# Optimization experiments

Hardware: AMD Instinct MI355X
Metric: run time of the kernel (lower is better)

## Reference

```python
import jax, jax.numpy as jnp
import numpy as np
import math

NUM_HEADS = 16
NUM_BUCKETS = 32
MAX_DISTANCE = 128
ALPHA = 32.0


def _rel_bucket(rel_pos):
    # bidirectional T5-style bucketing
    nb = NUM_BUCKETS // 2
    buckets = (rel_pos > 0).astype(jnp.int32) * nb
    rel_pos = jnp.abs(rel_pos)
    max_exact = nb // 2
    is_small = rel_pos < max_exact
    large = max_exact + (
        jnp.log(rel_pos.astype(jnp.float32) / max_exact + 1e-06)
        / math.log(MAX_DISTANCE / max_exact)
        * (nb - max_exact)
    ).astype(jnp.int32)
    large = jnp.minimum(large, nb - 1)
    return buckets + jnp.where(is_small, rel_pos, large)


def setup_inputs() -> dict:
    key = jax.random.key(0)
    ks = jax.random.split(key, 12)
    T, B, E = 1024, 4, 1024
    hd = E // NUM_HEADS
    s = 0.02
    f32 = jnp.float32
    return {
        "query": jax.random.normal(ks[0], (T, B, E), f32),
        "q_w": jax.random.normal(ks[1], (E, E), f32) * s,
        "q_b": jnp.zeros((E,), f32),
        "k_w": jax.random.normal(ks[2], (E, E), f32) * s,
        "k_b": jnp.zeros((E,), f32),
        "v_w": jax.random.normal(ks[3], (E, E), f32) * s,
        "v_b": jnp.zeros((E,), f32),
        "out_w": jax.random.normal(ks[4], (E, E), f32) * s,
        "out_b": jnp.zeros((E,), f32),
        "rel_emb": jax.random.normal(ks[5], (NUM_BUCKETS, NUM_HEADS), f32) * 0.1,
        "grep_w": jax.random.normal(ks[6], (hd, 8), f32) * s,
        "grep_b": jnp.zeros((8,), f32),
        "grep_a": jnp.ones((1, NUM_HEADS, 1, 1), f32),
        "bias_k": jax.random.normal(ks[7], (1, 1, E), f32) * s,
        "bias_v": jax.random.normal(ks[8], (1, 1, E), f32) * s,
    }


def reference(query, q_w, q_b, k_w, k_b, v_w, v_b, out_w, out_b,
              rel_emb, grep_w, grep_b, grep_a, bias_k, bias_v):
    tgt_len, bsz, embed_dim = query.shape
    nh = NUM_HEADS
    hd = embed_dim // nh
    scaling = hd ** (-0.5)

    # projections (self-attention: q, k, v all from query)
    q = query @ q_w + q_b
    k = query @ k_w + k_b
    v = query @ v_w + v_b
    q = q * scaling / ALPHA

    # bias_kv concat along sequence axis
    k = jnp.concatenate([k, jnp.tile(bias_k, (1, bsz, 1))], axis=0)
    v = jnp.concatenate([v, jnp.tile(bias_v, (1, bsz, 1))], axis=0)

    # faithful to source layout (including its (bsz,tgt,nh,hd)->(bsz*nh,tgt,hd) reshape)
    q = jnp.transpose(q.reshape(tgt_len, bsz, nh, hd), (1, 0, 2, 3)).reshape(bsz * nh, tgt_len, hd)
    k = jnp.transpose(k.reshape(-1, bsz, nh, hd), (1, 0, 2, 3)).reshape(bsz * nh, -1, hd)
    v = jnp.transpose(v.reshape(-1, bsz, nh, hd), (1, 0, 2, 3)).reshape(bsz * nh, -1, hd)
    src_len = k.shape[1]

    # [B*H, T, S]
    attn_weights = jnp.einsum("bth,bsh->bts", q, k)

    # T5-style relative position bias
    rel_pos = jnp.arange(src_len)[None, :] - jnp.arange(tgt_len)[:, None]
    buckets = _rel_bucket(rel_pos)                        # [T, S]
    pb = rel_emb[buckets]                                 # [T, S, H]
    pb = jnp.transpose(pb, (2, 0, 1))                     # [H, T, S]
    pb = jnp.tile(pb[None], (bsz, 1, 1, 1)).reshape(bsz * nh, tgt_len, src_len)

    # GRU-style gating of the position bias
    query_layer = q.reshape(bsz, nh, tgt_len, hd) * ALPHA / scaling
    gate = jax.nn.sigmoid((query_layer @ grep_w + grep_b).sum(-1, keepdims=True))
    gate = (gate * grep_a).reshape(bsz * nh, tgt_len, 1)
    attn_weights = attn_weights + gate * pb

    probs = jax.nn.softmax(attn_weights, axis=-1)
    attn = jnp.einsum("bts,bsh->bth", probs, v)           # [B*H, T, hd]
    attn = attn.reshape(bsz, nh, tgt_len, hd)
    attn = jnp.transpose(attn, (2, 0, 1, 3)).reshape(tgt_len, bsz, embed_dim)
    return attn @ out_w + out_b
```

## Files before the change

kernel.cpp:

```cpp
#include <hip/hip_runtime.h>
#include <stdint.h>

typedef unsigned short u16;
typedef unsigned int   u32;
typedef __attribute__((ext_vector_type(4)))  float f32x4;
typedef __attribute__((ext_vector_type(16))) float f32x16;
typedef __attribute__((ext_vector_type(8)))  short short8;
typedef __attribute__((ext_vector_type(8)))  u16   u16x8;
typedef __attribute__((ext_vector_type(4)))  u16   u16x4;
typedef __attribute__((ext_vector_type(4)))  u32   u32x4;
typedef __attribute__((ext_vector_type(4)))  float fv4;

#define T_LEN 1024
#define EMB   1024
#define SPAD  1088
#define LOG2E 1.44269504f

#define OFF_QX   (0ull)
#define OFF_VT   (0ull)
#define OFF_WT   (8912896ull)
#define OFF_QB   (17301504ull)
#define OFF_KB   (25690112ull)
#define OFF_VB   (34603008ull)
#define OFF_AT   (34603008ull)
#define OFF_GATE (43515904ull)
#define OFF_PB   (43778048ull)
#define OFF_AUX  (43909120ull)

__device__ __forceinline__ u16 f2bf(float f) {
  uint32_t u = __builtin_bit_cast(uint32_t, f);
  u += 0x7FFFu + ((u >> 16) & 1u);
  return (u16)(u >> 16);
}
__device__ __forceinline__ float bf2f(u16 s) {
  uint32_t u = ((uint32_t)s) << 16;
  return __builtin_bit_cast(float, u);
}
__device__ __forceinline__ void gld_lds16(const void* gp, void* lp) {
  __builtin_amdgcn_global_load_lds(
      (const __attribute__((address_space(1))) uint32_t*)(uintptr_t)(gp),
      (__attribute__((address_space(3))) uint32_t*)(uintptr_t)(lp),
      16, 0, 0);
}

__global__ void k_convert_q(const float* __restrict__ q, u16* __restrict__ qx) {
  int i = blockIdx.x * 256 + threadIdx.x;
  fv4 v = *((const fv4*)q + i);
  u16x4 o = { f2bf(v[0]), f2bf(v[1]), f2bf(v[2]), f2bf(v[3]) };
  *((u16x4*)qx + i) = o;
}

__global__ void k_transw(const float* __restrict__ w0, const float* __restrict__ w1,
                         const float* __restrict__ w2, const float* __restrict__ w3,
                         u16* __restrict__ wt) {
  __shared__ float tile[32][33];
  const int z = blockIdx.z;
  const float* w = (z == 0) ? w0 : (z == 1) ? w1 : (z == 2) ? w2 : w3;
  const int r0 = blockIdx.y * 32, c0 = blockIdx.x * 32;
  const int tx = threadIdx.x, ty = threadIdx.y;
  #pragma unroll
  for (int j = 0; j < 32; j += 8)
    tile[ty + j][tx] = w[(size_t)(r0 + ty + j) * EMB + c0 + tx];
  __syncthreads();
  u16* o = wt + (size_t)z * EMB * EMB;
  #pragma unroll
  for (int j = 0; j < 32; j += 8)
    o[(size_t)(c0 + ty + j) * EMB + r0 + tx] = f2bf(tile[tx][ty + j]);
}

__global__ void k_pb(const float* __restrict__ rel_emb, float* __restrict__ pbtab,
                     const float* __restrict__ grep_w, const float* __restrict__ grep_b,
                     float* __restrict__ aux) {
  int i = blockIdx.x * 256 + threadIdx.x;
  int rel = 1024 - i;
  int bucket = (rel > 0) ? 16 : 0;
  int r = rel < 0 ? -rel : rel;
  int bidx;
  if (r < 8) bidx = r;
  else {
    float lf = __logf((float)r / 8.0f + 1e-6f) * (1.0f / logf(16.0f)) * 8.0f;
    int large = 8 + (int)lf;
    bidx = large < 15 ? large : 15;
  }
  bucket += bidx;
  #pragma unroll
  for (int h = 0; h < 16; ++h) pbtab[h * 2048 + i] = rel_emb[bucket * 16 + h] * LOG2E;
  if (blockIdx.x == 0) {
    if (threadIdx.x < 64) {
      float s = 0.f;
      #pragma unroll
      for (int j = 0; j < 8; ++j) s += grep_w[threadIdx.x * 8 + j];
      aux[threadIdx.x] = s;
    } else if (threadIdx.x == 64) {
      float s = 0.f;
      #pragma unroll
      for (int j = 0; j < 8; ++j) s += grep_b[j];
      aux[64] = s;
    }
  }
}

__device__ __forceinline__ void gemm_tile(const u16* __restrict__ A, const u16* __restrict__ Bt,
                                          int m0, int n0, u16* As, u16* Bs, f32x4 acc[4][4]) {
  const int tid = threadIdx.x;
  const int lane = tid & 63, wid = tid >> 6;
  const int wm = wid >> 1, wn = wid & 1;
  const int l15 = lane & 15, l4 = lane >> 4;
  for (int kt = 0; kt < EMB; kt += 32) {
    #pragma unroll
    for (int i = 0; i < 2; ++i) {
      int cw = wid * 64 + i * 256;
      int c = cw + lane;
      int row = c >> 2, cb = c & 3;
      gld_lds16(A  + (size_t)(m0 + row) * EMB + kt + cb * 8, (char*)As + (size_t)cw * 16);
      gld_lds16(Bt + (size_t)(n0 + row) * EMB + kt + cb * 8, (char*)Bs + (size_t)cw * 16);
    }
    __syncthreads();
    short8 a[4], b[4];
    #pragma unroll
    for (int f = 0; f < 4; ++f) {
      a[f] = *(const short8*)(As + (wm * 64 + f * 16 + l15) * 32 + l4 * 8);
      b[f] = *(const short8*)(Bs + (wn * 64 + f * 16 + l15) * 32 + l4 * 8);
    }
    #pragma unroll
    for (int mi = 0; mi < 4; ++mi)
      #pragma unroll
      for (int ni = 0; ni < 4; ++ni)
        acc[mi][ni] = __builtin_amdgcn_mfma_f32_16x16x32_bf16(a[mi], b[ni], acc[mi][ni], 0, 0, 0);
    __syncthreads();
  }
}

__global__ __launch_bounds__(256, 2) void k_qkv_gemm(const u16* __restrict__ qx, const u16* __restrict__ wt,
    const float* __restrict__ qbias, const float* __restrict__ kbias, const float* __restrict__ vbias,
    u16* __restrict__ qb, u16* __restrict__ kb, u16* __restrict__ vb) {
  __shared__ u16 lds[8192];
  f32x4 acc[4][4];
  #pragma unroll
  for (int i = 0; i < 4; ++i)
    #pragma unroll
    for (int j = 0; j < 4; ++j) acc[i][j] = (f32x4){0.f, 0.f, 0.f, 0.f};
  const int m0 = blockIdx.y * 128, n0g = blockIdx.x * 128;
  gemm_tile(qx, wt, m0, n0g, lds, lds + 4096, acc);
  const int z = n0g >> 10;
  const float* bias = (z == 0) ? qbias : (z == 1) ? kbias : vbias;
  const int lane = threadIdx.x & 63, wid = threadIdx.x >> 6;
  const int wm = wid >> 1, wn = wid & 1, l15 = lane & 15, l4 = lane >> 4;
  #pragma unroll
  for (int ni = 0; ni < 4; ++ni) {
    int colg = n0g + wn * 64 + ni * 16 + l15;
    int col = colg & 1023;
    float bv = bias[col];
    int h = col >> 6, d = col & 63;
    #pragma unroll
    for (int mi = 0; mi < 4; ++mi) {
      #pragma unroll
      for (int r = 0; r < 4; ++r) {
        int row = m0 + wm * 64 + mi * 16 + l4 * 4 + r;
        int t = row >> 2, b = row & 3;
        float v = acc[mi][ni][r] + bv;
        if (z == 0) {
          int x = b * 16 + (t >> 6), u = ((t & 63) << 4) + h;
          qb[((size_t)x * 1024 + u) * 64 + d] = f2bf(v * (LOG2E / 256.0f));
        } else {
          int w = t * 16 + h;
          int j = w / 1025;
          int u = w - j * 1025;
          int x = b * 16 + j;
          if (z == 1) kb[((size_t)x * SPAD + u) * 64 + d] = f2bf(v);
          else        vb[((size_t)x * SPAD + u) * 64 + d] = f2bf(v);
        }
      }
    }
  }
}

__global__ void k_biaskv(const float* __restrict__ bias_k, const float* __restrict__ bias_v,
                         u16* __restrict__ kb, u16* __restrict__ vb) {
  int i = blockIdx.x * 256 + threadIdx.x;
  int b = i >> 10, h = (i >> 6) & 15, d = i & 63;
  int x = b * 16 + 15, u = 1009 + h;
  kb[((size_t)x * SPAD + u) * 64 + d] = f2bf(bias_k[h * 64 + d]);
  vb[((size_t)x * SPAD + u) * 64 + d] = f2bf(bias_v[h * 64 + d]);
}

__global__ void k_vtrans(const u16* __restrict__ vb, u16* __restrict__ vt) {
  __shared__ u16 t[64][72];
  const int x = blockIdx.y;
  const int u0 = blockIdx.x * 64;
  const int tid = threadIdx.x;
  const int ur = tid >> 2, c0 = (tid & 3) * 16;
  const u16* src = vb + ((size_t)x * SPAD + u0 + ur) * 64 + c0;
  u16x8 a0 = *(const u16x8*)(src);
  u16x8 a1 = *(const u16x8*)(src + 8);
  *(u16x8*)(&t[ur][c0]) = a0;
  *(u16x8*)(&t[ur][c0 + 8]) = a1;
  __syncthreads();
  const int d = tid >> 2, j = tid & 3;
  u16x8 o0, o1;
  #pragma unroll
  for (int i = 0; i < 8; ++i) o0[i] = t[j * 16 + i][d];
  #pragma unroll
  for (int i = 0; i < 8; ++i) o1[i] = t[j * 16 + 8 + i][d];
  u16* dst = vt + ((size_t)x * 64 + d) * SPAD + u0 + j * 16;
  *(u16x8*)(dst) = o0;
  *(u16x8*)(dst + 8) = o1;
}

__global__ void k_gate(const u16* __restrict__ qb, const float* __restrict__ aux,
                       const float* __restrict__ grep_a, float* __restrict__ gate) {
  int tid = threadIdx.x, lane = tid & 63, wid = tid >> 6;
  int row0 = (blockIdx.x * 4 + wid) * 8;
  int sub = lane >> 3, d0 = (lane & 7) * 8;
  int item = row0 + sub;
  u16x8 q8 = *(const u16x8*)(qb + (size_t)item * 64 + d0);
  float acc = 0.f;
  #pragma unroll
  for (int j = 0; j < 8; ++j) acc += bf2f(q8[j]) * aux[d0 + j];
  acc += __shfl_xor(acc, 1);
  acc += __shfl_xor(acc, 2);
  acc += __shfl_xor(acc, 4);
  if ((lane & 7) == 0) {
    float v = acc * (256.0f / LOG2E) + aux[64];
    float s = 1.0f / (1.0f + __expf(-v));
    gate[item] = s * grep_a[(item >> 10) & 15];
  }
}

__global__ __launch_bounds__(256, 2) void k_attn(const u16* __restrict__ qb, const u16* __restrict__ kb,
    const u16* __restrict__ vt, const float* __restrict__ gate, const float* __restrict__ pbt,
    u16* __restrict__ at) {
  __shared__ float pb_s[2048];
  const int tid = threadIdx.x, lane = tid & 63, wid = tid >> 6;
  const int l31 = lane & 31, l5 = lane >> 5;
  const int bid = blockIdx.x;
  const int x = (bid & 7) + ((bid >> 6) << 3);
  const int tblk = (bid >> 3) & 7;
  const int h = x & 15, b = x >> 4;
  const int T = tblk * 128 + wid * 32 + l31;

  #pragma unroll
  for (int i = 0; i < 2; ++i) {
    int idx = (tid + i * 256) * 4;
    *(fv4*)(pb_s + idx) = *(const fv4*)(pbt + (size_t)h * 2048 + idx);
  }

  short8 qf[4];
  #pragma unroll
  for (int c = 0; c < 4; ++c)
    qf[c] = *(const short8*)(qb + ((size_t)x * 1024 + T) * 64 + c * 16 + l5 * 8);
  const float g = gate[(size_t)x * 1024 + T];

  const u16* kbx = kb + (size_t)x * SPAD * 64;
  const u16* vtx = vt + (size_t)x * 64 * SPAD;

  f32x16 O0 = {}, O1 = {};
  float lsum = 0.f;
  __syncthreads();

  for (int ic = 0; ic < 16; ++ic) {
    const int s0 = ic * 64;
    short8 ka[2][4];
    #pragma unroll
    for (int ss = 0; ss < 2; ++ss)
      #pragma unroll
      for (int c = 0; c < 4; ++c)
        ka[ss][c] = *(const short8*)(kbx + (size_t)(s0 + ss * 32 + l31) * 64 + c * 16 + l5 * 8);
    f32x16 sc0 = {}, sc1 = {};
    #pragma unroll
    for (int c = 0; c < 4; ++c) {
      sc0 = __builtin_amdgcn_mfma_f32_32x32x16_bf16(ka[0][c], qf[c], sc0, 0, 0, 0);
      sc1 = __builtin_amdgcn_mfma_f32_32x32x16_bf16(ka[1][c], qf[c], sc1, 0, 0, 0);
    }
    short8 va[2][4];
    #pragma unroll
    for (int ds = 0; ds < 2; ++ds)
      #pragma unroll
      for (int c = 0; c < 4; ++c)
        va[ds][c] = *(const short8*)(vtx + (size_t)(ds * 32 + l31) * SPAD + s0 + c * 16 + l5 * 8);

    const int base = 1024 + T - s0;
    u32 pk[16];
    #pragma unroll
    for (int r = 0; r < 16; r += 2) {
      int soff = (r & 3) + 8 * (r >> 2) + 4 * l5;
      float p0 = exp2f(sc0[r]     + g * pb_s[base - soff]);
      float p1 = exp2f(sc0[r + 1] + g * pb_s[base - soff - 1]);
      lsum += p0 + p1;
      pk[r >> 1] = (__builtin_bit_cast(u32, p1) & 0xFFFF0000u) |
                   (__builtin_bit_cast(u32, p0) >> 16);
    }
    #pragma unroll
    for (int r = 0; r < 16; r += 2) {
      int soff = 32 + (r & 3) + 8 * (r >> 2) + 4 * l5;
      float p0 = exp2f(sc1[r]     + g * pb_s[base - soff]);
      float p1 = exp2f(sc1[r + 1] + g * pb_s[base - soff - 1]);
      lsum += p0 + p1;
      pk[8 + (r >> 1)] = (__builtin_bit_cast(u32, p1) & 0xFFFF0000u) |
                         (__builtin_bit_cast(u32, p0) >> 16);
    }

    const bool lo = (l5 == 0);
    #pragma unroll
    for (int ss = 0; ss < 2; ++ss) {
      u32 X0 = (u32)__shfl_xor((int)pk[ss * 8 + 0], 32);
      u32 X1 = (u32)__shfl_xor((int)pk[ss * 8 + 1], 32);
      u32 X2 = (u32)__shfl_xor((int)pk[ss * 8 + 2], 32);
      u32 X3 = (u32)__shfl_xor((int)pk[ss * 8 + 3], 32);
      u32x4 f0 = { lo ? pk[ss * 8 + 0] : X2, lo ? pk[ss * 8 + 1] : X3,
                   lo ? X0 : pk[ss * 8 + 2], lo ? X1 : pk[ss * 8 + 3] };
      short8 pf0 = __builtin_bit_cast(short8, f0);
      O0 = __builtin_amdgcn_mfma_f32_32x32x16_bf16(va[0][ss * 2], pf0, O0, 0, 0, 0);
      O1 = __builtin_amdgcn_mfma_f32_32x32x16_bf16(va[1][ss * 2], pf0, O1, 0, 0, 0);
      u32 Y0 = (u32)__shfl_xor((int)pk[ss * 8 + 4], 32);
      u32 Y1 = (u32)__shfl_xor((int)pk[ss * 8 + 5], 32);
      u32 Y2 = (u32)__shfl_xor((int)pk[ss * 8 + 6], 32);
      u32 Y3 = (u32)__shfl_xor((int)pk[ss * 8 + 7], 32);
      u32x4 f1 = { lo ? pk[ss * 8 + 4] : Y2, lo ? pk[ss * 8 + 5] : Y3,
                   lo ? Y0 : pk[ss * 8 + 6], lo ? Y1 : pk[ss * 8 + 7] };
      short8 pf1 = __builtin_bit_cast(short8, f1);
      O0 = __builtin_amdgcn_mfma_f32_32x32x16_bf16(va[0][ss * 2 + 1], pf1, O0, 0, 0, 0);
      O1 = __builtin_amdgcn_mfma_f32_32x32x16_bf16(va[1][ss * 2 + 1], pf1, O1, 0, 0, 0);
    }
  }

  float dot = 0.f;
  #pragma unroll
  for (int c = 0; c < 4; ++c) {
    short8 kt = *(const short8*)(kbx + (size_t)1024 * 64 + c * 16 + l5 * 8);
    #pragma unroll
    for (int j = 0; j < 8; ++j)
      dot += bf2f((u16)qf[c][j]) * bf2f((u16)kt[j]);
  }
  dot += __shfl_xor(dot, 32);
  float se = dot + g * pb_s[T];
  float p_t = exp2f(se);
  lsum += __shfl_xor(lsum, 32);
  float linv = 1.0f / (lsum + p_t);

  #pragma unroll
  for (int ds = 0; ds < 2; ++ds) {
    #pragma unroll
    for (int q2 = 0; q2 < 4; ++q2) {
      int d0 = ds * 32 + q2 * 8 + l5 * 4;
      u16x4 ov;
      #pragma unroll
      for (int e = 0; e < 4; ++e) {
        float vtl = bf2f(vtx[(size_t)(d0 + e) * SPAD + 1024]);
        float o = ((ds ? O1[q2 * 4 + e] : O0[q2 * 4 + e]) + p_t * vtl) * linv;
        ov[e] = f2bf(o);
      }
      *(u16x4*)(at + ((size_t)(T * 4 + b)) * 1024 + h * 64 + d0) = ov;
    }
  }
}

__global__ __launch_bounds__(256, 2) void k_out_gemm(const u16* __restrict__ at, const u16* __restrict__ wt3,
                                                     const float* __restrict__ obias, float* __restrict__ out) {
  __shared__ u16 lds[8192];
  f32x4 acc[4][4];
  #pragma unroll
  for (int i = 0; i < 4; ++i)
    #pragma unroll
    for (int j = 0; j < 4; ++j) acc[i][j] = (f32x4){0.f, 0.f, 0.f, 0.f};
  const int m0 = blockIdx.y * 128, n0 = blockIdx.x * 128;
  gemm_tile(at, wt3, m0, n0, lds, lds + 4096, acc);
  const int lane = threadIdx.x & 63, wid = threadIdx.x >> 6;
  const int wm = wid >> 1, wn = wid & 1, l15 = lane & 15, l4 = lane >> 4;
  #pragma unroll
  for (int ni = 0; ni < 4; ++ni) {
    int col = n0 + wn * 64 + ni * 16 + l15;
    float bv = obias[col];
    #pragma unroll
    for (int mi = 0; mi < 4; ++mi) {
      #pragma unroll
      for (int r = 0; r < 4; ++r) {
        int row = m0 + wm * 64 + mi * 16 + l4 * 4 + r;
        out[(size_t)row * 1024 + col] = acc[mi][ni][r] + bv;
      }
    }
  }
}

extern "C" void kernel_launch(void* const* d_in, const int* in_sizes, int n_in,
                              void* d_out, int out_size, void* d_ws, size_t ws_size,
                              hipStream_t stream) {
  const float* query   = (const float*)d_in[0];
  const float* q_w     = (const float*)d_in[1];
  const float* q_b     = (const float*)d_in[2];
  const float* k_w     = (const float*)d_in[3];
  const float* k_b     = (const float*)d_in[4];
  const float* v_w     = (const float*)d_in[5];
  const float* v_b     = (const float*)d_in[6];
  const float* out_w   = (const float*)d_in[7];
  const float* out_b   = (const float*)d_in[8];
  const float* rel_emb = (const float*)d_in[9];
  const float* grep_w  = (const float*)d_in[10];
  const float* grep_b  = (const float*)d_in[11];
  const float* grep_a  = (const float*)d_in[12];
  const float* bias_k  = (const float*)d_in[13];
  const float* bias_v  = (const float*)d_in[14];
  char* ws = (char*)d_ws;
  u16*   qx  = (u16*)(ws + OFF_QX);
  u16*   vt  = (u16*)(ws + OFF_VT);
  u16*   wt  = (u16*)(ws + OFF_WT);
  u16*   qb  = (u16*)(ws + OFF_QB);
  u16*   kb  = (u16*)(ws + OFF_KB);
  u16*   vb  = (u16*)(ws + OFF_VB);
  u16*   at  = (u16*)(ws + OFF_AT);
  float* gate = (float*)(ws + OFF_GATE);
  float* pbt  = (float*)(ws + OFF_PB);
  float* aux  = (float*)(ws + OFF_AUX);
  float* out  = (float*)d_out;

  k_convert_q<<<dim3(4096), dim3(256), 0, stream>>>(query, qx);
  k_transw<<<dim3(32, 32, 4), dim3(32, 8), 0, stream>>>(q_w, k_w, v_w, out_w, wt);
  k_pb<<<dim3(8), dim3(256), 0, stream>>>(rel_emb, pbt, grep_w, grep_b, aux);
  k_qkv_gemm<<<dim3(24, 32), dim3(256), 0, stream>>>(qx, wt, q_b, k_b, v_b, qb, kb, vb);
  k_biaskv<<<dim3(16), dim3(256), 0, stream>>>(bias_k, bias_v, kb, vb);
  k_vtrans<<<dim3(17, 64), dim3(256), 0, stream>>>(vb, vt);
  k_gate<<<dim3(2048), dim3(256), 0, stream>>>(qb, aux, grep_a, gate);
  k_attn<<<dim3(512), dim3(256), 0, stream>>>(qb, kb, vt, gate, pbt, at);
  k_out_gemm<<<dim3(8, 32), dim3(256), 0, stream>>>(at, wt + (size_t)3 * EMB * EMB, out_b, out);
}
```

Baseline: 248.9 us.

## Merge prep and mid kernels, prefetch K in attention, use permlane32 swap

Three small setup kernels are merged into one launch, and bias_kv insertion, V transpose and gate computation are merged into another, which cuts the launch count from nine to five. The attention loop now double-buffers K fragments so the next chunk's loads are issued ahead of the current MFMAs. It also wraps the MFMA sections in s_setprio and replaces the shfl_xor-plus-select exchange with v_permlane32_swap. The trade-off is higher register pressure from the prefetch buffers, plus a bias_v overwrite that now depends on an index range inside the transpose.

```diff
diff --git a/kernel.cpp b/kernel.cpp
--- a/kernel.cpp
+++ b/kernel.cpp
@@ -43,59 +43,61 @@
       16, 0, 0);
 }
 
-__global__ void k_convert_q(const float* __restrict__ q, u16* __restrict__ qx) {
-  int i = blockIdx.x * 256 + threadIdx.x;
-  fv4 v = *((const fv4*)q + i);
-  u16x4 o = { f2bf(v[0]), f2bf(v[1]), f2bf(v[2]), f2bf(v[3]) };
-  *((u16x4*)qx + i) = o;
-}
-
-__global__ void k_transw(const float* __restrict__ w0, const float* __restrict__ w1,
-                         const float* __restrict__ w2, const float* __restrict__ w3,
-                         u16* __restrict__ wt) {
+__global__ void k_prep(const float* __restrict__ q, u16* __restrict__ qx,
+                       const float* __restrict__ w0, const float* __restrict__ w1,
+                       const float* __restrict__ w2, const float* __restrict__ w3,
+                       u16* __restrict__ wt,
+                       const float* __restrict__ rel_emb, float* __restrict__ pbtab,
+                       const float* __restrict__ grep_w, const float* __restrict__ grep_b,
+                       float* __restrict__ aux) {
   __shared__ float tile[32][33];
-  const int z = blockIdx.z;
-  const float* w = (z == 0) ? w0 : (z == 1) ? w1 : (z == 2) ? w2 : w3;
-  const int r0 = blockIdx.y * 32, c0 = blockIdx.x * 32;
-  const int tx = threadIdx.x, ty = threadIdx.y;
-  #pragma unroll
-  for (int j = 0; j < 32; j += 8)
-    tile[ty + j][tx] = w[(size_t)(r0 + ty + j) * EMB + c0 + tx];
-  __syncthreads();
-  u16* o = wt + (size_t)z * EMB * EMB;
-  #pragma unroll
-  for (int j = 0; j < 32; j += 8)
-    o[(size_t)(c0 + ty + j) * EMB + r0 + tx] = f2bf(tile[tx][ty + j]);
-}
-
-__global__ void k_pb(const float* __restrict__ rel_emb, float* __restrict__ pbtab,
-                     const float* __restrict__ grep_w, const float* __restrict__ grep_b,
-                     float* __restrict__ aux) {
-  int i = blockIdx.x * 256 + threadIdx.x;
-  int rel = 1024 - i;
-  int bucket = (rel > 0) ? 16 : 0;
-  int r = rel < 0 ? -rel : rel;
-  int bidx;
-  if (r < 8) bidx = r;
-  else {
-    float lf = __logf((float)r / 8.0f + 1e-6f) * (1.0f / logf(16.0f)) * 8.0f;
-    int large = 8 + (int)lf;
-    bidx = large < 15 ? large : 15;
-  }
-  bucket += bidx;
-  #pragma unroll
-  for (int h = 0; h < 16; ++h) pbtab[h * 2048 + i] = rel_emb[bucket * 16 + h] * LOG2E;
-  if (blockIdx.x == 0) {
-    if (threadIdx.x < 64) {
-      float s = 0.f;
-      #pragma unroll
-      for (int j = 0; j < 8; ++j) s += grep_w[threadIdx.x * 8 + j];
-      aux[threadIdx.x] = s;
-    } else if (threadIdx.x == 64) {
-      float s = 0.f;
-      #pragma unroll
-      for (int j = 0; j < 8; ++j) s += grep_b[j];
-      aux[64] = s;
+  const int bid = blockIdx.x, tid = threadIdx.x;
+  if (bid < 4096) {
+    int i = bid * 256 + tid;
+    fv4 v = *((const fv4*)q + i);
+    u16x4 o = { f2bf(v[0]), f2bf(v[1]), f2bf(v[2]), f2bf(v[3]) };
+    *((u16x4*)qx + i) = o;
+  } else if (bid < 8192) {
+    int b2 = bid - 4096;
+    int z = b2 >> 10, xy = b2 & 1023;
+    int r0 = (xy >> 5) * 32, c0 = (xy & 31) * 32;
+    const float* w = (z == 0) ? w0 : (z == 1) ? w1 : (z == 2) ? w2 : w3;
+    int tx = tid & 31, ty = tid >> 5;
+    #pragma unroll
+    for (int j = 0; j < 32; j += 8)
+      tile[ty + j][tx] = w[(size_t)(r0 + ty + j) * EMB + c0 + tx];
+    __syncthreads();
+    u16* o = wt + (size_t)z * EMB * EMB;
+    #pragma unroll
+    for (int j = 0; j < 32; j += 8)
+      o[(size_t)(c0 + ty + j) * EMB + r0 + tx] = f2bf(tile[tx][ty + j]);
+  } else {
+    int i = (bid - 8192) * 256 + tid;
+    int rel = 1024 - i;
+    int bucket = (rel > 0) ? 16 : 0;
+    int r = rel < 0 ? -rel : rel;
+    int bidx;
+    if (r < 8) bidx = r;
+    else {
+      float lf = __logf((float)r / 8.0f + 1e-6f) * (1.0f / logf(16.0f)) * 8.0f;
+      int large = 8 + (int)lf;
+      bidx = large < 15 ? large : 15;
+    }
+    bucket += bidx;
+    #pragma unroll
+    for (int hh = 0; hh < 16; ++hh) pbtab[hh * 2048 + i] = rel_emb[bucket * 16 + hh] * LOG2E;
+    if (bid == 8192) {
+      if (tid < 64) {
+        float s = 0.f;
+        #pragma unroll
+        for (int j = 0; j < 8; ++j) s += grep_w[tid * 8 + j];
+        aux[tid] = s;
+      } else if (tid == 64) {
+        float s = 0.f;
+        #pragma unroll
+        for (int j = 0; j < 8; ++j) s += grep_b[j];
+        aux[64] = s;
+      }
     }
   }
 }
@@ -175,55 +177,63 @@
   }
 }
 
-__global__ void k_biaskv(const float* __restrict__ bias_k, const float* __restrict__ bias_v,
-                         u16* __restrict__ kb, u16* __restrict__ vb) {
-  int i = blockIdx.x * 256 + threadIdx.x;
-  int b = i >> 10, h = (i >> 6) & 15, d = i & 63;
-  int x = b * 16 + 15, u = 1009 + h;
-  kb[((size_t)x * SPAD + u) * 64 + d] = f2bf(bias_k[h * 64 + d]);
-  vb[((size_t)x * SPAD + u) * 64 + d] = f2bf(bias_v[h * 64 + d]);
-}
-
-__global__ void k_vtrans(const u16* __restrict__ vb, u16* __restrict__ vt) {
+__global__ void k_mid(const u16* __restrict__ vb, u16* __restrict__ vt, u16* __restrict__ kb,
+                      const float* __restrict__ bias_k, const float* __restrict__ bias_v,
+                      const u16* __restrict__ qb, const float* __restrict__ aux,
+                      const float* __restrict__ grep_a, float* __restrict__ gate) {
   __shared__ u16 t[64][72];
-  const int x = blockIdx.y;
-  const int u0 = blockIdx.x * 64;
-  const int tid = threadIdx.x;
-  const int ur = tid >> 2, c0 = (tid & 3) * 16;
-  const u16* src = vb + ((size_t)x * SPAD + u0 + ur) * 64 + c0;
-  u16x8 a0 = *(const u16x8*)(src);
-  u16x8 a1 = *(const u16x8*)(src + 8);
-  *(u16x8*)(&t[ur][c0]) = a0;
-  *(u16x8*)(&t[ur][c0 + 8]) = a1;
-  __syncthreads();
-  const int d = tid >> 2, j = tid & 3;
-  u16x8 o0, o1;
-  #pragma unroll
-  for (int i = 0; i < 8; ++i) o0[i] = t[j * 16 + i][d];
-  #pragma unroll
-  for (int i = 0; i < 8; ++i) o1[i] = t[j * 16 + 8 + i][d];
-  u16* dst = vt + ((size_t)x * 64 + d) * SPAD + u0 + j * 16;
-  *(u16x8*)(dst) = o0;
-  *(u16x8*)(dst + 8) = o1;
-}
-
-__global__ void k_gate(const u16* __restrict__ qb, const float* __restrict__ aux,
-                       const float* __restrict__ grep_a, float* __restrict__ gate) {
-  int tid = threadIdx.x, lane = tid & 63, wid = tid >> 6;
-  int row0 = (blockIdx.x * 4 + wid) * 8;
-  int sub = lane >> 3, d0 = (lane & 7) * 8;
-  int item = row0 + sub;
-  u16x8 q8 = *(const u16x8*)(qb + (size_t)item * 64 + d0);
-  float acc = 0.f;
-  #pragma unroll
-  for (int j = 0; j < 8; ++j) acc += bf2f(q8[j]) * aux[d0 + j];
-  acc += __shfl_xor(acc, 1);
-  acc += __shfl_xor(acc, 2);
-  acc += __shfl_xor(acc, 4);
-  if ((lane & 7) == 0) {
-    float v = acc * (256.0f / LOG2E) + aux[64];
-    float s = 1.0f / (1.0f + __expf(-v));
-    gate[item] = s * grep_a[(item >> 10) & 15];
+  const int bid = blockIdx.x, tid = threadIdx.x;
+  if (bid < 1088) {
+    const int x = bid / 17, uc = bid - (bid / 17) * 17;
+    const int u0 = uc * 64;
+    const int ur = tid >> 2, c0 = (tid & 3) * 16;
+    const u16* src = vb + ((size_t)x * SPAD + u0 + ur) * 64 + c0;
+    u16x8 a0 = *(const u16x8*)(src);
+    u16x8 a1 = *(const u16x8*)(src + 8);
+    const int ug = u0 + ur;
+    if ((x & 15) == 15 && ug >= 1009 && ug <= 1024) {
+      const float* bs = bias_v + (ug - 1009) * 64 + c0;
+      #pragma unroll
+      for (int i = 0; i < 8; ++i) { a0[i] = f2bf(bs[i]); a1[i] = f2bf(bs[8 + i]); }
+    }
+    *(u16x8*)(&t[ur][c0]) = a0;
+    *(u16x8*)(&t[ur][c0 + 8]) = a1;
+    __syncthreads();
+    const int d = tid >> 2, j = tid & 3;
+    u16x8 o0, o1;
+    #pragma unroll
+    for (int i = 0; i < 8; ++i) o0[i] = t[j * 16 + i][d];
+    #pragma unroll
+    for (int i = 0; i < 8; ++i) o1[i] = t[j * 16 + 8 + i][d];
+    u16* dst = vt + ((size_t)x * 64 + d) * SPAD + u0 + j * 16;
+    *(u16x8*)(dst) = o0;
+    *(u16x8*)(dst + 8) = o1;
+    if ((x & 15) == 15 && uc == 16) {
+      int k = tid * 4;
+      int hh = k >> 6, dd = k & 63;
+      u16x4 kv;
+      #pragma unroll
+      for (int e = 0; e < 4; ++e) kv[e] = f2bf(bias_k[hh * 64 + dd + e]);
+      *(u16x4*)(kb + ((size_t)x * SPAD + 1009 + hh) * 64 + dd) = kv;
+    }
+  } else {
+    int gb = bid - 1088;
+    int lane = tid & 63, wid = tid >> 6;
+    int row0 = (gb * 4 + wid) * 8;
+    int sub = lane >> 3, d0 = (lane & 7) * 8;
+    int item = row0 + sub;
+    u16x8 q8 = *(const u16x8*)(qb + (size_t)item * 64 + d0);
+    float acc = 0.f;
+    #pragma unroll
+    for (int j = 0; j < 8; ++j) acc += bf2f(q8[j]) * aux[d0 + j];
+    acc += __shfl_xor(acc, 1);
+    acc += __shfl_xor(acc, 2);
+    acc += __shfl_xor(acc, 4);
+    if ((lane & 7) == 0) {
+      float v = acc * (256.0f / LOG2E) + aux[64];
+      float s = 1.0f / (1.0f + __expf(-v));
+      gate[item] = s * grep_a[(item >> 10) & 15];
+    }
   }
 }
 
@@ -256,29 +266,39 @@
 
   f32x16 O0 = {}, O1 = {};
   float lsum = 0.f;
+
+  short8 kA[2][4], kB[2][4];
+  #pragma unroll
+  for (int ss = 0; ss < 2; ++ss)
+    #pragma unroll
+    for (int c = 0; c < 4; ++c)
+      kA[ss][c] = *(const short8*)(kbx + (size_t)(ss * 32 + l31) * 64 + c * 16 + l5 * 8);
   __syncthreads();
 
-  for (int ic = 0; ic < 16; ++ic) {
+  auto step = [&](short8 (&ka)[2][4], short8 (&kn)[2][4], int ic, bool pf) {
     const int s0 = ic * 64;
-    short8 ka[2][4];
-    #pragma unroll
-    for (int ss = 0; ss < 2; ++ss)
+    short8 va[2][4];
+    #pragma unroll
+    for (int ds = 0; ds < 2; ++ds)
       #pragma unroll
       for (int c = 0; c < 4; ++c)
-        ka[ss][c] = *(const short8*)(kbx + (size_t)(s0 + ss * 32 + l31) * 64 + c * 16 + l5 * 8);
+        va[ds][c] = *(const short8*)(vtx + (size_t)(ds * 32 + l31) * SPAD + s0 + c * 16 + l5 * 8);
+    if (pf) {
+      const int sn = s0 + 64;
+      #pragma unroll
+      for (int ss = 0; ss < 2; ++ss)
+        #pragma unroll
+        for (int c = 0; c < 4; ++c)
+          kn[ss][c] = *(const short8*)(kbx + (size_t)(sn + ss * 32 + l31) * 64 + c * 16 + l5 * 8);
+    }
     f32x16 sc0 = {}, sc1 = {};
+    __builtin_amdgcn_s_setprio(1);
     #pragma unroll
     for (int c = 0; c < 4; ++c) {
       sc0 = __builtin_amdgcn_mfma_f32_32x32x16_bf16(ka[0][c], qf[c], sc0, 0, 0, 0);
       sc1 = __builtin_amdgcn_mfma_f32_32x32x16_bf16(ka[1][c], qf[c], sc1, 0, 0, 0);
     }
-    short8 va[2][4];
-    #pragma unroll
-    for (int ds = 0; ds < 2; ++ds)
-      #pragma unroll
-      for (int c = 0; c < 4; ++c)
-        va[ds][c] = *(const short8*)(vtx + (size_t)(ds * 32 + l31) * SPAD + s0 + c * 16 + l5 * 8);
-
+    __builtin_amdgcn_s_setprio(0);
     const int base = 1024 + T - s0;
     u32 pk[16];
     #pragma unroll
@@ -299,29 +319,33 @@
       pk[8 + (r >> 1)] = (__builtin_bit_cast(u32, p1) & 0xFFFF0000u) |
                          (__builtin_bit_cast(u32, p0) >> 16);
     }
-
-    const bool lo = (l5 == 0);
+    __builtin_amdgcn_s_setprio(1);
     #pragma unroll
     for (int ss = 0; ss < 2; ++ss) {
-      u32 X0 = (u32)__shfl_xor((int)pk[ss * 8 + 0], 32);
-      u32 X1 = (u32)__shfl_xor((int)pk[ss * 8 + 1], 32);
-      u32 X2 = (u32)__shfl_xor((int)pk[ss * 8 + 2], 32);
-      u32 X3 = (u32)__shfl_xor((int)pk[ss * 8 + 3], 32);
-      u32x4 f0 = { lo ? pk[ss * 8 + 0] : X2, lo ? pk[ss * 8 + 1] : X3,
-                   lo ? X0 : pk[ss * 8 + 2], lo ? X1 : pk[ss * 8 + 3] };
-      short8 pf0 = __builtin_bit_cast(short8, f0);
+      u32 a0 = pk[ss * 8 + 0], a1 = pk[ss * 8 + 1];
+      u32 b0 = pk[ss * 8 + 2], b1 = pk[ss * 8 + 3];
+      asm volatile("v_permlane32_swap_b32 %0, %1" : "+v"(a0), "+v"(b0));
+      asm volatile("v_permlane32_swap_b32 %0, %1" : "+v"(a1), "+v"(b1));
+      u32x4 f0v = { a0, a1, b0, b1 };
+      short8 pf0 = __builtin_bit_cast(short8, f0v);
       O0 = __builtin_amdgcn_mfma_f32_32x32x16_bf16(va[0][ss * 2], pf0, O0, 0, 0, 0);
       O1 = __builtin_amdgcn_mfma_f32_32x32x16_bf16(va[1][ss * 2], pf0, O1, 0, 0, 0);
-      u32 Y0 = (u32)__shfl_xor((int)pk[ss * 8 + 4], 32);
-      u32 Y1 = (u32)__shfl_xor((int)pk[ss * 8 + 5], 32);
-      u32 Y2 = (u32)__shfl_xor((int)pk[ss * 8 + 6], 32);
-      u32 Y3 = (u32)__shfl_xor((int)pk[ss * 8 + 7], 32);
-      u32x4 f1 = { lo ? pk[ss * 8 + 4] : Y2, lo ? pk[ss * 8 + 5] : Y3,
-                   lo ? Y0 : pk[ss * 8 + 6], lo ? Y1 : pk[ss * 8 + 7] };
-      short8 pf1 = __builtin_bit_cast(short8, f1);
+      u32 c0 = pk[ss * 8 + 4], c1 = pk[ss * 8 + 5];
+      u32 d0 = pk[ss * 8 + 6], d1 = pk[ss * 8 + 7];
+      asm volatile("v_permlane32_swap_b32 %0, %1" : "+v"(c0), "+v"(d0));
+      asm volatile("v_permlane32_swap_b32 %0, %1" : "+v"(c1), "+v"(d1));
+      u32x4 f1v = { c0, c1, d0, d1 };
+      short8 pf1 = __builtin_bit_cast(short8, f1v);
       O0 = __builtin_amdgcn_mfma_f32_32x32x16_bf16(va[0][ss * 2 + 1], pf1, O0, 0, 0, 0);
       O1 = __builtin_amdgcn_mfma_f32_32x32x16_bf16(va[1][ss * 2 + 1], pf1, O1, 0, 0, 0);
     }
+    __builtin_amdgcn_s_setprio(0);
+  };
+
+  #pragma unroll 1
+  for (int ic = 0; ic < 16; ic += 2) {
+    step(kA, kB, ic, true);
+    step(kB, kA, ic + 1, ic + 1 < 15);
   }
 
   float dot = 0.f;
@@ -413,13 +437,10 @@
   float* aux  = (float*)(ws + OFF_AUX);
   float* out  = (float*)d_out;
 
-  k_convert_q<<<dim3(4096), dim3(256), 0, stream>>>(query, qx);
-  k_transw<<<dim3(32, 32, 4), dim3(32, 8), 0, stream>>>(q_w, k_w, v_w, out_w, wt);
-  k_pb<<<dim3(8), dim3(256), 0, stream>>>(rel_emb, pbt, grep_w, grep_b, aux);
+  k_prep<<<dim3(8200), dim3(256), 0, stream>>>(query, qx, q_w, k_w, v_w, out_w, wt,
+                                               rel_emb, pbt, grep_w, grep_b, aux);
   k_qkv_gemm<<<dim3(24, 32), dim3(256), 0, stream>>>(qx, wt, q_b, k_b, v_b, qb, kb, vb);
-  k_biaskv<<<dim3(16), dim3(256), 0, stream>>>(bias_k, bias_v, kb, vb);
-  k_vtrans<<<dim3(17, 64), dim3(256), 0, stream>>>(vb, vt);
-  k_gate<<<dim3(2048), dim3(256), 0, stream>>>(qb, aux, grep_a, gate);
+  k_mid<<<dim3(3136), dim3(256), 0, stream>>>(vb, vt, kb, bias_k, bias_v, qb, aux, grep_a, gate);
   k_attn<<<dim3(512), dim3(256), 0, stream>>>(qb, kb, vt, gate, pbt, at);
   k_out_gemm<<<dim3(8, 32), dim3(256), 0, stream>>>(at, wt + (size_t)3 * EMB * EMB, out_b, out);
 }
```

New measurement: 234.4 us. 1.06x faster.
